# Performance work log

Hardware: AMD Instinct MI355X
Metric: run time of the kernel (lower is better)

Reference implementation:

```python
import jax, jax.numpy as jnp
import numpy as np

# 5 standard YOLOv2 anchors (w, h) in grid units
ANCHORS = np.array([[0.57273, 0.677385], [1.87446, 2.06253], [3.33843, 5.47434],
                    [7.88282, 3.52778], [9.77052, 9.16828]], dtype=np.float32)
NA = 5
OBJECT_SCALE = 5.0
NO_OBJECT_SCALE = 1.0
COORD_SCALE = 1.0
SIL_THRESH = 0.6


def bbox_iou(b1, b2):
    """IoU for center-format boxes; b1/b2 are (x, y, w, h) tuples of broadcastable arrays."""
    x1, y1, w1, h1 = b1
    x2, y2, w2, h2 = b2
    mx = jnp.minimum(x1 - w1 * 0.5, x2 - w2 * 0.5)
    Mx = jnp.maximum(x1 + w1 * 0.5, x2 + w2 * 0.5)
    my = jnp.minimum(y1 - h1 * 0.5, y2 - h2 * 0.5)
    My = jnp.maximum(y1 + h1 * 0.5, y2 + h2 * 0.5)
    cw = w1 + w2 - (Mx - mx)  # intersection width
    ch = h1 + h2 - (My - my)  # intersection height
    carea = jnp.where((cw <= 0) | (ch <= 0), 0.0, cw * ch)
    uarea = w1 * h1 + w2 * h2 - carea
    return carea / uarea


def setup_inputs() -> dict:
    key = jax.random.key(0)
    k1, k2 = jax.random.split(key)
    pred = jax.random.normal(k1, (512, NA * 5, 76, 76), dtype=jnp.float32)
    # normalized gt boxes in (0,1); clip so grid indices stay in range and w,h > 0
    target = jnp.clip(jax.random.uniform(k2, (512, 4), dtype=jnp.float32), 1e-3, 0.999)
    return {"pred": pred, "target": target}


def reference(pred, target):
    bs, _, H, W = pred.shape  # H == W asserted in original
    dt = pred.dtype
    pred = pred.reshape(bs, NA, 5, H, W)
    anc = jnp.asarray(ANCHORS)

    # activations (pred_boxes: sigmoid on x,y; raw w,h; sigmoid conf)
    sx = jax.nn.sigmoid(pred[:, :, 0])
    sy = jax.nn.sigmoid(pred[:, :, 1])
    pw = pred[:, :, 2]
    ph = pred[:, :, 3]
    pconf = jax.nn.sigmoid(pred[:, :, 4])

    # grid-offset boxes (detached in original)
    gj_grid, gi_grid = jnp.meshgrid(jnp.arange(H, dtype=dt), jnp.arange(W, dtype=dt), indexing='ij')
    bx = jax.lax.stop_gradient(sx) + gi_grid
    by = jax.lax.stop_gradient(sy) + gj_grid
    bw = jnp.exp(jax.lax.stop_gradient(pw)) * anc[:, 0].reshape(1, NA, 1, 1)
    bh = jnp.exp(jax.lax.stop_gradient(ph)) * anc[:, 1].reshape(1, NA, 1, 1)

    tgt = jax.lax.stop_gradient(target)
    gx = tgt[:, 0] * W
    gy = tgt[:, 1] * H
    gw = tgt[:, 2] * W
    gh = tgt[:, 3] * H

    # conf mask: no_object_scale everywhere, 0 where IoU(gt, pred) > sil_thresh
    bc = lambda v: v.reshape(bs, 1, 1, 1)
    iou_all = bbox_iou((bc(gx), bc(gy), bc(gw), bc(gh)), (bx, by, bw, bh))  # (bs, NA, H, W)
    conf_mask = jnp.where(iou_all > SIL_THRESH, 0.0, NO_OBJECT_SCALE).astype(dt)

    # best anchor per batch element (wh-only IoU at origin)
    z_b = jnp.zeros((bs, 1), dt)
    z_a = jnp.zeros((1, NA), dt)
    iou_anc = bbox_iou((z_b, z_b, gw[:, None], gh[:, None]),
                       (z_a, z_a, anc[None, :, 0], anc[None, :, 1]))  # (bs, NA)
    best = jnp.argmax(iou_anc, axis=1)

    gi = gx.astype(jnp.int32)
    gj = gy.astype(jnp.int32)
    bidx = jnp.arange(bs)

    # IoU between gt and the matched predicted box
    pb = (bx[bidx, best, gj, gi], by[bidx, best, gj, gi],
          bw[bidx, best, gj, gi], bh[bidx, best, gj, gi])
    iou_t = bbox_iou((gx, gy, gw, gh), pb)

    # scatter target assignment (epoch == 0 branch of original: coord_mask=1, xy target base 0.5)
    conf_mask = conf_mask.at[bidx, best, gj, gi].set(OBJECT_SCALE)
    coord_mask = jnp.ones((bs, NA, H, W), dt)
    bahw = (bs, NA, H, W)
    tb_x = jnp.full(bahw, 0.5, dt).at[bidx, best, gj, gi].set(gx - gi.astype(dt))
    tb_y = jnp.full(bahw, 0.5, dt).at[bidx, best, gj, gi].set(gy - gj.astype(dt))
    tb_w = jnp.zeros(bahw, dt).at[bidx, best, gj, gi].set(jnp.log(gw / anc[best, 0]))
    tb_h = jnp.zeros(bahw, dt).at[bidx, best, gj, gi].set(jnp.log(gh / anc[best, 1]))
    tconf = jnp.zeros(bahw, dt).at[bidx, best, gj, gi].set(iou_t)

    cm = jnp.sqrt(conf_mask)
    sse = lambda a, b: jnp.sum((a - b) ** 2)
    loss_x = COORD_SCALE * sse(sx * coord_mask, tb_x * coord_mask) / 2.0
    loss_y = COORD_SCALE * sse(sy * coord_mask, tb_y * coord_mask) / 2.0
    loss_w = COORD_SCALE * sse(pw * coord_mask, tb_w * coord_mask) / 2.0
    loss_h = COORD_SCALE * sse(ph * coord_mask, tb_h * coord_mask) / 2.0
    loss_conf = sse(pconf * cm, tconf * cm) / 2.0
    loss = loss_x + loss_y + loss_w + loss_h + loss_conf
    return (loss, loss_x, loss_y, loss_w, loss_h, loss_conf)
```

## Files before the change

kernel.cpp:

```cpp
#include <hip/hip_runtime.h>
#include <math.h>

#define NA 5
#define HH 76
#define WW 76
#define HWSZ (HH * WW)
#define HW4 (HWSZ / 4)
#define NBLK (512 * NA)
#define OBJECT_SCALE 5.0f
#define SIL_THRESH 0.6f

#define PART_OFF 8192

__constant__ float ANC_W[NA] = {0.57273f, 1.87446f, 3.33843f, 7.88282f, 9.77052f};
__constant__ float ANC_H[NA] = {0.677385f, 2.06253f, 5.47434f, 3.52778f, 9.16828f};

typedef float v4f __attribute__((ext_vector_type(4)));

__device__ __forceinline__ float frcp(float x) { return __builtin_amdgcn_rcpf(x); }
__device__ __forceinline__ float sigm_fast(float x) { return frcp(1.0f + __expf(-x)); }

__global__ __launch_bounds__(256, 4) void
region_loss_main(const float* __restrict__ pred, const float* __restrict__ target,
                 float* __restrict__ ws) {
    const int ba = blockIdx.x;
    const int b  = ba / NA;
    const int a  = ba - b * NA;

    const float gx = target[b * 4 + 0] * (float)WW;
    const float gy = target[b * 4 + 1] * (float)HH;
    const float gw = target[b * 4 + 2] * (float)WW;
    const float gh = target[b * 4 + 3] * (float)HH;
    int best = 0;
    {
        float bestv = -1.0f;
#pragma unroll
        for (int aa = 0; aa < NA; ++aa) {
            float aw = ANC_W[aa], ah = ANC_H[aa];
            float inter = fminf(gw, aw) * fminf(gh, ah);
            float uni = gw * gh + aw * ah - inter;
            float iou = inter / uni;
            if (iou > bestv) { bestv = iou; best = aa; }
        }
    }
    const int gi = (int)gx;
    const int gj = (int)gy;
    const float tx_s = gx - (float)gi;
    const float ty_s = gy - (float)gj;
    const float tw_s = logf(gw / ANC_W[best]);
    const float th_s = logf(gh / ANC_H[best]);

    const float anw = ANC_W[a], anh = ANC_H[a];
    const bool anchit = (a == best);
    const float gxm = gx - gw * 0.5f, gxM = gx + gw * 0.5f;
    const float gym = gy - gh * 0.5f, gyM = gy + gh * 0.5f;
    const float garea = gw * gh;
    const float c_lo = logf(0.6f * garea / (anw * anh)) - 1e-3f;
    const float c_hi = c_lo + 1.0216512f + 2e-3f;

    const float* base = pred + (size_t)ba * 5 * HWSZ;
    float ax = 0.f, ay = 0.f, aw_ = 0.f, ah_ = 0.f, ac = 0.f;

    auto compute = [&](int r, v4f px, v4f py, v4f pw, v4f ph, v4f pc) {
        const int e0 = r * 4;
        const int j  = r / 19;
        const int i0 = e0 - j * WW;
        const bool rowhit = anchit && (j == gj) && (gi >= i0) && (gi < i0 + 4);
#pragma unroll
        for (int k = 0; k < 4; ++k) {
            float sx = sigm_fast(px[k]);
            float sy = sigm_fast(py[k]);
            float sc = sigm_fast(pc[k]);
            const bool special = rowhit && ((i0 + k) == gi);

            float cmask = 1.0f, tconf = 0.0f;
            const float t = pw[k] + ph[k];
            if (((t > c_lo) & (t < c_hi)) | special) {
                float bw = __expf(pw[k]) * anw;
                float bh = __expf(ph[k]) * anh;
                float bx = sx + (float)(i0 + k);
                float by = sy + (float)j;
                float mx = fminf(gxm, bx - bw * 0.5f);
                float Mx = fmaxf(gxM, bx + bw * 0.5f);
                float my = fminf(gym, by - bh * 0.5f);
                float My = fmaxf(gyM, by + bh * 0.5f);
                float cw = gw + bw - (Mx - mx);
                float ch = gh + bh - (My - my);
                float carea = (cw <= 0.f || ch <= 0.f) ? 0.f : cw * ch;
                float uarea = garea + bw * bh - carea;
                float iou = carea * frcp(uarea);
                cmask = (iou > SIL_THRESH) ? 0.f : 1.f;
                if (special) { cmask = OBJECT_SCALE; tconf = iou; }
            }

            float tx = special ? tx_s : 0.5f;
            float ty = special ? ty_s : 0.5f;
            float tw = special ? tw_s : 0.0f;
            float th = special ? th_s : 0.0f;
            float dx = sx - tx, dy = sy - ty;
            float dw = pw[k] - tw, dh = ph[k] - th;
            float dc = sc - tconf;
            ax += dx * dx;
            ay += dy * dy;
            aw_ += dw * dw;
            ah_ += dh * dh;
            ac += cmask * dc * dc;
        }
    };

    int r = threadIdx.x;
    for (; r + 256 < HW4; r += 512) {
        const int r2 = r + 256;
        v4f px0 = __builtin_nontemporal_load((const v4f*)(base + r * 4));
        v4f py0 = __builtin_nontemporal_load((const v4f*)(base + HWSZ + r * 4));
        v4f pw0 = __builtin_nontemporal_load((const v4f*)(base + 2 * HWSZ + r * 4));
        v4f ph0 = __builtin_nontemporal_load((const v4f*)(base + 3 * HWSZ + r * 4));
        v4f pc0 = __builtin_nontemporal_load((const v4f*)(base + 4 * HWSZ + r * 4));
        v4f px1 = __builtin_nontemporal_load((const v4f*)(base + r2 * 4));
        v4f py1 = __builtin_nontemporal_load((const v4f*)(base + HWSZ + r2 * 4));
        v4f pw1 = __builtin_nontemporal_load((const v4f*)(base + 2 * HWSZ + r2 * 4));
        v4f ph1 = __builtin_nontemporal_load((const v4f*)(base + 3 * HWSZ + r2 * 4));
        v4f pc1 = __builtin_nontemporal_load((const v4f*)(base + 4 * HWSZ + r2 * 4));
        compute(r, px0, py0, pw0, ph0, pc0);
        compute(r2, px1, py1, pw1, ph1, pc1);
    }
    for (; r < HW4; r += 256) {
        v4f px = __builtin_nontemporal_load((const v4f*)(base + r * 4));
        v4f py = __builtin_nontemporal_load((const v4f*)(base + HWSZ + r * 4));
        v4f pw = __builtin_nontemporal_load((const v4f*)(base + 2 * HWSZ + r * 4));
        v4f ph = __builtin_nontemporal_load((const v4f*)(base + 3 * HWSZ + r * 4));
        v4f pc = __builtin_nontemporal_load((const v4f*)(base + 4 * HWSZ + r * 4));
        compute(r, px, py, pw, ph, pc);
    }

    __shared__ float sred[4][5];
    int lane = threadIdx.x & 63;
    int wid  = threadIdx.x >> 6;
    float vals[5] = {ax, ay, aw_, ah_, ac};
#pragma unroll
    for (int v = 0; v < 5; ++v) {
        float x = vals[v];
#pragma unroll
        for (int off = 32; off > 0; off >>= 1) x += __shfl_down(x, off, 64);
        if (lane == 0) sred[wid][v] = x;
    }
    __syncthreads();
    if (threadIdx.x < 5) {
        float s = sred[0][threadIdx.x] + sred[1][threadIdx.x] +
                  sred[2][threadIdx.x] + sred[3][threadIdx.x];
        ws[PART_OFF + blockIdx.x * 8 + threadIdx.x] = s;
    }
}

__global__ __launch_bounds__(256) void
reduce_finish(const float* __restrict__ ws, float* __restrict__ out) {
    float s0 = 0.f, s1 = 0.f, s2 = 0.f, s3 = 0.f, s4 = 0.f;
    for (int i = threadIdx.x; i < NBLK; i += 256) {
        const float* p = ws + PART_OFF + i * 8;
        s0 += p[0]; s1 += p[1]; s2 += p[2]; s3 += p[3]; s4 += p[4];
    }
    __shared__ float sred[4][5];
    int lane = threadIdx.x & 63;
    int wid  = threadIdx.x >> 6;
    float vals[5] = {s0, s1, s2, s3, s4};
#pragma unroll
    for (int v = 0; v < 5; ++v) {
        float x = vals[v];
#pragma unroll
        for (int off = 32; off > 0; off >>= 1) x += __shfl_down(x, off, 64);
        if (lane == 0) sred[wid][v] = x;
    }
    __syncthreads();
    if (threadIdx.x == 0) {
        float lx = (sred[0][0] + sred[1][0] + sred[2][0] + sred[3][0]) * 0.5f;
        float ly = (sred[0][1] + sred[1][1] + sred[2][1] + sred[3][1]) * 0.5f;
        float lw = (sred[0][2] + sred[1][2] + sred[2][2] + sred[3][2]) * 0.5f;
        float lh = (sred[0][3] + sred[1][3] + sred[2][3] + sred[3][3]) * 0.5f;
        float lc = (sred[0][4] + sred[1][4] + sred[2][4] + sred[3][4]) * 0.5f;
        out[0] = lx + ly + lw + lh + lc;
        out[1] = lx;
        out[2] = ly;
        out[3] = lw;
        out[4] = lh;
        out[5] = lc;
    }
}

extern "C" void kernel_launch(void* const* d_in, const int* in_sizes, int n_in,
                              void* d_out, int out_size, void* d_ws, size_t ws_size,
                              hipStream_t stream) {
    const float* pred   = (const float*)d_in[0];
    const float* target = (const float*)d_in[1];
    float* ws  = (float*)d_ws;
    float* out = (float*)d_out;
    int bs = in_sizes[1] / 4;

    region_loss_main<<<bs * NA, 256, 0, stream>>>(pred, target, ws);
    reduce_finish<<<1, 256, 0, stream>>>(ws, out);
}
```

Measured before the change: 372.3 us.

## Use persistent 1024-block grid over half-slices and fuse final reduction via atomic counter

Splits each (batch, anchor) slice into two halves and has a fixed grid of 1024 blocks process five half-slice tasks each, balancing work across CUs instead of launching 2560 blocks. The separate finishing kernel is removed: the last block to arrive, detected through an atomic counter in workspace, performs the final reduction. This saves a kernel launch but adds a memset launch and per-task setup recomputation. The hardcoded grid and task count assume batch size 512.

```diff
diff --git a/kernel.cpp b/kernel.cpp
--- a/kernel.cpp
+++ b/kernel.cpp
@@ -6,7 +6,9 @@
 #define WW 76
 #define HWSZ (HH * WW)
 #define HW4 (HWSZ / 4)
-#define NBLK (512 * NA)
+#define HALF4 (HW4 / 2)
+#define GRID 1024
+#define NTASK (512 * NA * 2)
 #define OBJECT_SCALE 5.0f
 #define SIL_THRESH 0.6f
 
@@ -22,120 +24,128 @@
 
 __global__ __launch_bounds__(256, 4) void
 region_loss_main(const float* __restrict__ pred, const float* __restrict__ target,
-                 float* __restrict__ ws) {
-    const int ba = blockIdx.x;
-    const int b  = ba / NA;
-    const int a  = ba - b * NA;
-
-    const float gx = target[b * 4 + 0] * (float)WW;
-    const float gy = target[b * 4 + 1] * (float)HH;
-    const float gw = target[b * 4 + 2] * (float)WW;
-    const float gh = target[b * 4 + 3] * (float)HH;
-    int best = 0;
-    {
-        float bestv = -1.0f;
-#pragma unroll
-        for (int aa = 0; aa < NA; ++aa) {
-            float aw = ANC_W[aa], ah = ANC_H[aa];
-            float inter = fminf(gw, aw) * fminf(gh, ah);
-            float uni = gw * gh + aw * ah - inter;
-            float iou = inter / uni;
-            if (iou > bestv) { bestv = iou; best = aa; }
+                 float* __restrict__ ws, float* __restrict__ out) {
+    float ax = 0.f, ay = 0.f, aw_ = 0.f, ah_ = 0.f, ac = 0.f;
+
+    for (int it = 0; it < 5; ++it) {
+        const int t    = blockIdx.x + (it << 10);
+        const int ba   = t >> 1;
+        const int half = t & 1;
+        const int b    = ba / NA;
+        const int a    = ba - b * NA;
+
+        const float gx = target[b * 4 + 0] * (float)WW;
+        const float gy = target[b * 4 + 1] * (float)HH;
+        const float gw = target[b * 4 + 2] * (float)WW;
+        const float gh = target[b * 4 + 3] * (float)HH;
+        int best = 0;
+        {
+            float bestv = -1.0f;
+#pragma unroll
+            for (int aa = 0; aa < NA; ++aa) {
+                float aw = ANC_W[aa], ah = ANC_H[aa];
+                float inter = fminf(gw, aw) * fminf(gh, ah);
+                float uni = gw * gh + aw * ah - inter;
+                float iou = inter / uni;
+                if (iou > bestv) { bestv = iou; best = aa; }
+            }
         }
-    }
-    const int gi = (int)gx;
-    const int gj = (int)gy;
-    const float tx_s = gx - (float)gi;
-    const float ty_s = gy - (float)gj;
-    const float tw_s = logf(gw / ANC_W[best]);
-    const float th_s = logf(gh / ANC_H[best]);
-
-    const float anw = ANC_W[a], anh = ANC_H[a];
-    const bool anchit = (a == best);
-    const float gxm = gx - gw * 0.5f, gxM = gx + gw * 0.5f;
-    const float gym = gy - gh * 0.5f, gyM = gy + gh * 0.5f;
-    const float garea = gw * gh;
-    const float c_lo = logf(0.6f * garea / (anw * anh)) - 1e-3f;
-    const float c_hi = c_lo + 1.0216512f + 2e-3f;
-
-    const float* base = pred + (size_t)ba * 5 * HWSZ;
-    float ax = 0.f, ay = 0.f, aw_ = 0.f, ah_ = 0.f, ac = 0.f;
-
-    auto compute = [&](int r, v4f px, v4f py, v4f pw, v4f ph, v4f pc) {
-        const int e0 = r * 4;
-        const int j  = r / 19;
-        const int i0 = e0 - j * WW;
-        const bool rowhit = anchit && (j == gj) && (gi >= i0) && (gi < i0 + 4);
-#pragma unroll
-        for (int k = 0; k < 4; ++k) {
-            float sx = sigm_fast(px[k]);
-            float sy = sigm_fast(py[k]);
-            float sc = sigm_fast(pc[k]);
-            const bool special = rowhit && ((i0 + k) == gi);
-
-            float cmask = 1.0f, tconf = 0.0f;
-            const float t = pw[k] + ph[k];
-            if (((t > c_lo) & (t < c_hi)) | special) {
-                float bw = __expf(pw[k]) * anw;
-                float bh = __expf(ph[k]) * anh;
-                float bx = sx + (float)(i0 + k);
-                float by = sy + (float)j;
-                float mx = fminf(gxm, bx - bw * 0.5f);
-                float Mx = fmaxf(gxM, bx + bw * 0.5f);
-                float my = fminf(gym, by - bh * 0.5f);
-                float My = fmaxf(gyM, by + bh * 0.5f);
-                float cw = gw + bw - (Mx - mx);
-                float ch = gh + bh - (My - my);
-                float carea = (cw <= 0.f || ch <= 0.f) ? 0.f : cw * ch;
-                float uarea = garea + bw * bh - carea;
-                float iou = carea * frcp(uarea);
-                cmask = (iou > SIL_THRESH) ? 0.f : 1.f;
-                if (special) { cmask = OBJECT_SCALE; tconf = iou; }
+        const int gi = (int)gx;
+        const int gj = (int)gy;
+        const float tx_s = gx - (float)gi;
+        const float ty_s = gy - (float)gj;
+        const float tw_s = logf(gw / ANC_W[best]);
+        const float th_s = logf(gh / ANC_H[best]);
+
+        const float anw = ANC_W[a], anh = ANC_H[a];
+        const bool anchit = (a == best);
+        const float gxm = gx - gw * 0.5f, gxM = gx + gw * 0.5f;
+        const float gym = gy - gh * 0.5f, gyM = gy + gh * 0.5f;
+        const float garea = gw * gh;
+        const float c_lo = logf(0.6f * garea / (anw * anh)) - 1e-3f;
+        const float c_hi = c_lo + 1.0216512f + 2e-3f;
+
+        const float* base = pred + (size_t)ba * 5 * HWSZ;
+
+        auto compute = [&](int r, v4f px, v4f py, v4f pw, v4f ph, v4f pc) {
+            const int e0 = r * 4;
+            const int j  = r / 19;
+            const int i0 = e0 - j * WW;
+            const bool rowhit = anchit && (j == gj) && (gi >= i0) && (gi < i0 + 4);
+#pragma unroll
+            for (int k = 0; k < 4; ++k) {
+                float sx = sigm_fast(px[k]);
+                float sy = sigm_fast(py[k]);
+                float sc = sigm_fast(pc[k]);
+                const bool special = rowhit && ((i0 + k) == gi);
+
+                float cmask = 1.0f, tconf = 0.0f;
+                const float tt = pw[k] + ph[k];
+                if (((tt > c_lo) & (tt < c_hi)) | special) {
+                    float bw = __expf(pw[k]) * anw;
+                    float bh = __expf(ph[k]) * anh;
+                    float bx = sx + (float)(i0 + k);
+                    float by = sy + (float)j;
+                    float mx = fminf(gxm, bx - bw * 0.5f);
+                    float Mx = fmaxf(gxM, bx + bw * 0.5f);
+                    float my = fminf(gym, by - bh * 0.5f);
+                    float My = fmaxf(gyM, by + bh * 0.5f);
+                    float cw = gw + bw - (Mx - mx);
+                    float ch = gh + bh - (My - my);
+                    float carea = (cw <= 0.f || ch <= 0.f) ? 0.f : cw * ch;
+                    float uarea = garea + bw * bh - carea;
+                    float iou = carea * frcp(uarea);
+                    cmask = (iou > SIL_THRESH) ? 0.f : 1.f;
+                    if (special) { cmask = OBJECT_SCALE; tconf = iou; }
+                }
+
+                float tx = special ? tx_s : 0.5f;
+                float ty = special ? ty_s : 0.5f;
+                float tw = special ? tw_s : 0.0f;
+                float th = special ? th_s : 0.0f;
+                float dx = sx - tx, dy = sy - ty;
+                float dw = pw[k] - tw, dh = ph[k] - th;
+                float dc = sc - tconf;
+                ax += dx * dx;
+                ay += dy * dy;
+                aw_ += dw * dw;
+                ah_ += dh * dh;
+                ac += cmask * dc * dc;
             }
-
-            float tx = special ? tx_s : 0.5f;
-            float ty = special ? ty_s : 0.5f;
-            float tw = special ? tw_s : 0.0f;
-            float th = special ? th_s : 0.0f;
-            float dx = sx - tx, dy = sy - ty;
-            float dw = pw[k] - tw, dh = ph[k] - th;
-            float dc = sc - tconf;
-            ax += dx * dx;
-            ay += dy * dy;
-            aw_ += dw * dw;
-            ah_ += dh * dh;
-            ac += cmask * dc * dc;
+        };
+
+        const int rbeg = half * HALF4;
+        const int rend = rbeg + HALF4;
+        int r = rbeg + threadIdx.x;
+        for (; r + 256 < rend; r += 512) {
+            const int r2 = r + 256;
+            v4f px0 = __builtin_nontemporal_load((const v4f*)(base + r * 4));
+            v4f py0 = __builtin_nontemporal_load((const v4f*)(base + HWSZ + r * 4));
+            v4f pw0 = __builtin_nontemporal_load((const v4f*)(base + 2 * HWSZ + r * 4));
+            v4f ph0 = __builtin_nontemporal_load((const v4f*)(base + 3 * HWSZ + r * 4));
+            v4f pc0 = __builtin_nontemporal_load((const v4f*)(base + 4 * HWSZ + r * 4));
+            v4f px1 = __builtin_nontemporal_load((const v4f*)(base + r2 * 4));
+            v4f py1 = __builtin_nontemporal_load((const v4f*)(base + HWSZ + r2 * 4));
+            v4f pw1 = __builtin_nontemporal_load((const v4f*)(base + 2 * HWSZ + r2 * 4));
+            v4f ph1 = __builtin_nontemporal_load((const v4f*)(base + 3 * HWSZ + r2 * 4));
+            v4f pc1 = __builtin_nontemporal_load((const v4f*)(base + 4 * HWSZ + r2 * 4));
+            compute(r, px0, py0, pw0, ph0, pc0);
+            compute(r2, px1, py1, pw1, ph1, pc1);
         }
-    };
-
-    int r = threadIdx.x;
-    for (; r + 256 < HW4; r += 512) {
-        const int r2 = r + 256;
-        v4f px0 = __builtin_nontemporal_load((const v4f*)(base + r * 4));
-        v4f py0 = __builtin_nontemporal_load((const v4f*)(base + HWSZ + r * 4));
-        v4f pw0 = __builtin_nontemporal_load((const v4f*)(base + 2 * HWSZ + r * 4));
-        v4f ph0 = __builtin_nontemporal_load((const v4f*)(base + 3 * HWSZ + r * 4));
-        v4f pc0 = __builtin_nontemporal_load((const v4f*)(base + 4 * HWSZ + r * 4));
-        v4f px1 = __builtin_nontemporal_load((const v4f*)(base + r2 * 4));
-        v4f py1 = __builtin_nontemporal_load((const v4f*)(base + HWSZ + r2 * 4));
-        v4f pw1 = __builtin_nontemporal_load((const v4f*)(base + 2 * HWSZ + r2 * 4));
-        v4f ph1 = __builtin_nontemporal_load((const v4f*)(base + 3 * HWSZ + r2 * 4));
-        v4f pc1 = __builtin_nontemporal_load((const v4f*)(base + 4 * HWSZ + r2 * 4));
-        compute(r, px0, py0, pw0, ph0, pc0);
-        compute(r2, px1, py1, pw1, ph1, pc1);
-    }
-    for (; r < HW4; r += 256) {
-        v4f px = __builtin_nontemporal_load((const v4f*)(base + r * 4));
-        v4f py = __builtin_nontemporal_load((const v4f*)(base + HWSZ + r * 4));
-        v4f pw = __builtin_nontemporal_load((const v4f*)(base + 2 * HWSZ + r * 4));
-        v4f ph = __builtin_nontemporal_load((const v4f*)(base + 3 * HWSZ + r * 4));
-        v4f pc = __builtin_nontemporal_load((const v4f*)(base + 4 * HWSZ + r * 4));
-        compute(r, px, py, pw, ph, pc);
+        for (; r < rend; r += 256) {
+            v4f px = __builtin_nontemporal_load((const v4f*)(base + r * 4));
+            v4f py = __builtin_nontemporal_load((const v4f*)(base + HWSZ + r * 4));
+            v4f pw = __builtin_nontemporal_load((const v4f*)(base + 2 * HWSZ + r * 4));
+            v4f ph = __builtin_nontemporal_load((const v4f*)(base + 3 * HWSZ + r * 4));
+            v4f pc = __builtin_nontemporal_load((const v4f*)(base + 4 * HWSZ + r * 4));
+            compute(r, px, py, pw, ph, pc);
+        }
     }
 
     __shared__ float sred[4][5];
-    int lane = threadIdx.x & 63;
-    int wid  = threadIdx.x >> 6;
+    __shared__ int lastflag;
+    const int lane = threadIdx.x & 63;
+    const int wid  = threadIdx.x >> 6;
     float vals[5] = {ax, ay, aw_, ah_, ac};
 #pragma unroll
     for (int v = 0; v < 5; ++v) {
@@ -150,22 +160,27 @@
                   sred[2][threadIdx.x] + sred[3][threadIdx.x];
         ws[PART_OFF + blockIdx.x * 8 + threadIdx.x] = s;
     }
-}
-
-__global__ __launch_bounds__(256) void
-reduce_finish(const float* __restrict__ ws, float* __restrict__ out) {
+    __syncthreads();
+
+    if (threadIdx.x == 0) {
+        unsigned prev = __hip_atomic_fetch_add((unsigned*)ws, 1u,
+                                               __ATOMIC_ACQ_REL,
+                                               __HIP_MEMORY_SCOPE_AGENT);
+        lastflag = (prev == GRID - 1);
+    }
+    __syncthreads();
+    if (!lastflag) return;
+
+    __threadfence();
     float s0 = 0.f, s1 = 0.f, s2 = 0.f, s3 = 0.f, s4 = 0.f;
-    for (int i = threadIdx.x; i < NBLK; i += 256) {
+    for (int i = threadIdx.x; i < GRID; i += 256) {
         const float* p = ws + PART_OFF + i * 8;
         s0 += p[0]; s1 += p[1]; s2 += p[2]; s3 += p[3]; s4 += p[4];
     }
-    __shared__ float sred[4][5];
-    int lane = threadIdx.x & 63;
-    int wid  = threadIdx.x >> 6;
-    float vals[5] = {s0, s1, s2, s3, s4};
+    float fvals[5] = {s0, s1, s2, s3, s4};
 #pragma unroll
     for (int v = 0; v < 5; ++v) {
-        float x = vals[v];
+        float x = fvals[v];
 #pragma unroll
         for (int off = 32; off > 0; off >>= 1) x += __shfl_down(x, off, 64);
         if (lane == 0) sred[wid][v] = x;
@@ -193,8 +208,7 @@
     const float* target = (const float*)d_in[1];
     float* ws  = (float*)d_ws;
     float* out = (float*)d_out;
-    int bs = in_sizes[1] / 4;
-
-    region_loss_main<<<bs * NA, 256, 0, stream>>>(pred, target, ws);
-    reduce_finish<<<1, 256, 0, stream>>>(ws, out);
+
+    hipMemsetAsync(d_ws, 0, 4, stream);
+    region_loss_main<<<GRID, 256, 0, stream>>>(pred, target, ws, out);
 }
```

Result: slower. 414.7 us (+11.4%).
